# Performance work log

Hardware: AMD Instinct MI355X
Metric: run time of the kernel (lower is better)

Reference implementation:

```python
import jax, jax.numpy as jnp
from jax import lax
import numpy as np

# gate config (matches init_kwargs)
TOP_K = 8
N_GROUP = 8
TOPK_GROUP = 4
ROUTED_SCALING_FACTOR = 2.5
NORM_TOPK_PROB = True


def setup_inputs() -> dict:
    key = jax.random.key(0)
    k1, k2, k3 = jax.random.split(key, 3)
    B, S, H, E = 4, 4096, 4096, 256
    x = jax.random.normal(k1, (B, S, H), dtype=jnp.float32)
    weight = jax.random.normal(k2, (E, H), dtype=jnp.float32) * 0.02
    bias = jax.random.normal(k3, (E,), dtype=jnp.float32) * 0.01
    return {"x": x, "weight": weight, "bias": bias}


def reference(x, weight, bias):
    # gate logits: [B, S, E]
    gates = jnp.einsum('bsh,eh->bse', x, weight)
    scores = jax.nn.sigmoid(gates.astype(jnp.float32))
    orig_scores = scores
    s = scores + bias  # biased scores used only for selection

    B, S, E = s.shape
    if N_GROUP > 1:
        Eg = E // N_GROUP
        sg = s.reshape(B, S, N_GROUP, Eg)
        # group score = sum of top-2 expert scores within each group: [B, S, G]
        group_scores = lax.top_k(sg, 2)[0].sum(axis=-1)
        k_drop = N_GROUP - TOPK_GROUP
        # indices of the k_drop lowest-scoring groups
        drop_idx = lax.top_k(-group_scores, k_drop)[1]  # [B, S, k_drop]
        # keep mask over groups: [B, S, G]
        keep = ~jnp.any(drop_idx[..., :, None] == jnp.arange(N_GROUP), axis=-2)
        sg = jnp.where(keep[..., None], sg, 0.0)  # scatter_ 0.0 on dropped groups
        s = sg.reshape(B, S, E)

    # final top-k over masked, biased scores
    inds = lax.top_k(s, TOP_K)[1]  # [B, S, TOP_K]
    sel = jnp.take_along_axis(orig_scores, inds, axis=-1)  # unbiased scores
    if TOP_K > 1 and NORM_TOPK_PROB:
        sel = sel / (sel.sum(axis=-1, keepdims=True) + 1e-20)
    sel = sel * ROUTED_SCALING_FACTOR
    return (inds, sel)
```

## Files before the change

### kernel.cpp

```cpp
#include <hip/hip_runtime.h>
#include <hip/hip_bf16.h>
#include <math.h>
#include <stdint.h>

#define HDIM   4096
#define NEXP   256
#define TOPK   8
#define NGRP   8
#define NTOK   16384
#define KSPLIT 2
#define BM     64
#define BK     32
#define KCHUNKS (HDIM/BK)
#define NIT    ((HDIM/KSPLIT)/BK)
#define TAU    2.5e-5f
#define TAUG   5.0e-5f

typedef __attribute__((ext_vector_type(8))) short short8v;
typedef __attribute__((ext_vector_type(4))) float f32x4;

#define WS_WSPLIT  (2ull*NTOK*NEXP*4)
#define WS_CTR     (WS_WSPLIT + 4ull*1024*1024)
#define WS_LIST    (WS_CTR + 256)

__device__ inline void gload_lds16(const void* g, void* l) {
    __builtin_amdgcn_global_load_lds(
        (const __attribute__((address_space(1))) unsigned int*)g,
        (__attribute__((address_space(3))) unsigned int*)l, 16, 0, 0);
}

__device__ inline unsigned rtn16(unsigned u) {
    return (u + 0x7fffu + ((u >> 16) & 1u)) >> 16;
}

__global__ __launch_bounds__(256)
void convert_w(const float* __restrict__ w, unsigned short* __restrict__ wws)
{
    int gid  = blockIdx.x * 256 + threadIdx.x;
    int e    = gid >> 9;
    int cell = gid & 511;
    int kc = cell >> 2, kb = cell & 3;
    const float* src = w + (size_t)e * HDIM + cell * 8;
    float4 f0 = *(const float4*)src;
    float4 f1 = *(const float4*)(src + 4);
    float fs[8] = {f0.x,f0.y,f0.z,f0.w,f1.x,f1.y,f1.z,f1.w};
    unsigned hw[4], lw[4];
#pragma unroll
    for (int p = 0; p < 4; ++p) {
        unsigned u0 = __float_as_uint(fs[2*p]);
        unsigned u1 = __float_as_uint(fs[2*p+1]);
        unsigned h0 = rtn16(u0), h1 = rtn16(u1);
        float r0 = fs[2*p]   - __uint_as_float(h0 << 16);
        float r1 = fs[2*p+1] - __uint_as_float(h1 << 16);
        unsigned l0 = rtn16(__float_as_uint(r0));
        unsigned l1 = rtn16(__float_as_uint(r1));
        hw[p] = h0 | (h1 << 16);
        lw[p] = l0 | (l1 << 16);
    }
    size_t bh = ((size_t)(kc*2 + 0)*4 + kb)*2048 + e*8;
    size_t blo= ((size_t)(kc*2 + 1)*4 + kb)*2048 + e*8;
    *(uint4*)&wws[bh]  = make_uint4(hw[0],hw[1],hw[2],hw[3]);
    *(uint4*)&wws[blo] = make_uint4(lw[0],lw[1],lw[2],lw[3]);
}

__global__ __launch_bounds__(256, 2)
void gate_gemm(const float* __restrict__ x, const unsigned short* __restrict__ wws,
               float* __restrict__ partials)
{
    __shared__ uint4 ldsv[2560];
    char* lds = (char*)ldsv;
    const int t = threadIdx.x;
    const int wid = t >> 6, lane = t & 63;
    const int mb = blockIdx.x & 255, ks = blockIdx.x >> 8;
    const size_t m0 = (size_t)mb * BM;
    const int frow = lane & 15, fkb = lane >> 4;
    const int srow = t & 63, skb = t >> 6;

    f32x4 acc[4][4];
#pragma unroll
    for (int m = 0; m < 4; ++m)
#pragma unroll
        for (int n = 0; n < 4; ++n) acc[m][n] = (f32x4){0.f,0.f,0.f,0.f};

    const float* xrow = x + (m0 + srow) * HDIM + ks * (HDIM/KSPLIT) + skb * 8;
    const char* wbase = (const char*)wws + (size_t)(ks * (KCHUNKS/KSPLIT)) * 32768;

    float4 xa = *(const float4*)(xrow);
    float4 xb = *(const float4*)(xrow + 4);

    for (int it = 0; it < NIT; ++it) {
        __syncthreads();
        {
            float fs[8] = {xa.x,xa.y,xa.z,xa.w,xb.x,xb.y,xb.z,xb.w};
            unsigned hw[4], lw[4];
#pragma unroll
            for (int p = 0; p < 4; ++p) {
                unsigned u0 = __float_as_uint(fs[2*p]);
                unsigned u1 = __float_as_uint(fs[2*p+1]);
                hw[p] = (u0 >> 16) | (u1 & 0xffff0000u);
                float r0 = fs[2*p]   - __uint_as_float(u0 & 0xffff0000u);
                float r1 = fs[2*p+1] - __uint_as_float(u1 & 0xffff0000u);
                unsigned l0 = rtn16(__float_as_uint(r0));
                unsigned l1 = rtn16(__float_as_uint(r1));
                lw[p] = l0 | (l1 << 16);
            }
            *(uint4*)&lds[skb*1024 + srow*16]        = make_uint4(hw[0],hw[1],hw[2],hw[3]);
            *(uint4*)&lds[4096 + skb*1024 + srow*16] = make_uint4(lw[0],lw[1],lw[2],lw[3]);
        }
        {
            const char* wsrc = wbase + (size_t)it * 32768;
#pragma unroll
            for (int j = 0; j < 8; ++j) {
                int chunk = wid * 8 + j;
                gload_lds16(wsrc + chunk*1024 + lane*16, &lds[8192 + chunk*1024]);
            }
        }
        __syncthreads();
        if (it + 1 < NIT) {
            xa = *(const float4*)(xrow + (it+1)*BK);
            xb = *(const float4*)(xrow + (it+1)*BK + 4);
        }
        short8v ah[4], al[4];
#pragma unroll
        for (int m = 0; m < 4; ++m) {
            ah[m] = *(const short8v*)&lds[        fkb*1024 + (m*16+frow)*16];
            al[m] = *(const short8v*)&lds[4096 +  fkb*1024 + (m*16+frow)*16];
        }
#pragma unroll
        for (int n = 0; n < 4; ++n) {
            int col = wid*64 + n*16 + frow;
            short8v bh = *(const short8v*)&lds[8192 +         fkb*4096 + col*16];
            short8v bl = *(const short8v*)&lds[8192 + 16384 + fkb*4096 + col*16];
#pragma unroll
            for (int m = 0; m < 4; ++m)
                acc[m][n] = __builtin_amdgcn_mfma_f32_16x16x32_bf16(ah[m], bh, acc[m][n], 0,0,0);
#pragma unroll
            for (int m = 0; m < 4; ++m)
                acc[m][n] = __builtin_amdgcn_mfma_f32_16x16x32_bf16(ah[m], bl, acc[m][n], 0,0,0);
#pragma unroll
            for (int m = 0; m < 4; ++m)
                acc[m][n] = __builtin_amdgcn_mfma_f32_16x16x32_bf16(al[m], bh, acc[m][n], 0,0,0);
        }
    }
    float* pb = partials + (size_t)ks * NTOK * NEXP;
#pragma unroll
    for (int m = 0; m < 4; ++m)
#pragma unroll
        for (int n = 0; n < 4; ++n) {
            int col = wid*64 + n*16 + (lane & 15);
#pragma unroll
            for (int r = 0; r < 4; ++r) {
                size_t row = m0 + m*16 + (lane >> 4)*4 + r;
                pb[row*NEXP + col] = acc[m][n][r];
            }
        }
}

__device__ void wave_gate_topk(float* gb , float* ss ,
                               const float* __restrict__ bias, int lane, size_t tok,
                               float* __restrict__ oIdx, float* __restrict__ oVal,
                               unsigned* flagCtr, int* flagList)
{
    float bv[4]; int ce[4];
#pragma unroll
    for (int j = 0; j < 4; ++j) {
        int e = lane + 64*j;
        float s = 1.f / (1.f + expf(-gb[e]));
        float b = s + bias[e];
        ss[e] = s; gb[e] = b;
        bv[j] = b; ce[j] = e;
    }
    int g = lane >> 3;
    float4 gv = *(const float4*)(gb + g*32 + (lane & 7)*4);
    float a1 = fmaxf(gv.x,gv.y), a2 = fminf(gv.x,gv.y);
    float b1 = fmaxf(gv.z,gv.w), b2 = fminf(gv.z,gv.w);
    float m1 = fmaxf(a1,b1);
    float m2 = fmaxf(fminf(a1,b1), fmaxf(a2,b2));
#pragma unroll
    for (int off = 1; off < 8; off <<= 1) {
        float om1 = __shfl_xor(m1, off), om2 = __shfl_xor(m2, off);
        float n1 = fmaxf(m1, om1);
        float n2 = fmaxf(fminf(m1, om1), fmaxf(m2, om2));
        m1 = n1; m2 = n2;
    }
    float gs = m1 + m2;
    float gsc[8];
#pragma unroll
    for (int i = 0; i < 8; ++i) gsc[i] = __shfl(gs, i*8);
    unsigned dropped = 0; float lastdrop = 0.f;
#pragma unroll
    for (int itd = 0; itd < 4; ++itd) {
        float mn = 1e38f; int mi = 0;
#pragma unroll
        for (int i = 0; i < 8; ++i)
            if (!((dropped >> i) & 1) && gsc[i] < mn) { mn = gsc[i]; mi = i; }
        dropped |= 1u << mi; lastdrop = mn;
    }
    float minkeep = 1e38f;
#pragma unroll
    for (int i = 0; i < 8; ++i)
        if (!((dropped >> i) & 1)) minkeep = fminf(minkeep, gsc[i]);
    float gmargin = minkeep - lastdrop;

    float cv[4];
#pragma unroll
    for (int j = 0; j < 4; ++j)
        cv[j] = ((dropped >> (ce[j] >> 5)) & 1) ? 0.0f : bv[j];

    float vals[9]; int ind[9];
#pragma unroll
    for (int r = 0; r < 9; ++r) {
        float lv = -1e38f; int li = 0x7fffffff;
#pragma unroll
        for (int j = 0; j < 4; ++j)
            if (cv[j] > lv || (cv[j] == lv && ce[j] < li)) { lv = cv[j]; li = ce[j]; }
#pragma unroll
        for (int off = 32; off >= 1; off >>= 1) {
            float ov = __shfl_xor(lv, off);
            int   oi = __shfl_xor(li, off);
            if (ov > lv || (ov == lv && oi < li)) { lv = ov; li = oi; }
        }
        vals[r] = lv; ind[r] = li;
#pragma unroll
        for (int j = 0; j < 4; ++j)
            if (ce[j] == li) cv[j] = -1e38f;
    }
    float mingap = 1e38f;
#pragma unroll
    for (int r = 0; r < 8; ++r) mingap = fminf(mingap, vals[r] - vals[r+1]);

    int myi = 0;
#pragma unroll
    for (int r = 0; r < 8; ++r) if (lane == r) myi = ind[r];
    float sv = (lane < 8) ? ss[myi] : 0.f;
    float sum = sv;
#pragma unroll
    for (int off = 1; off < 8; off <<= 1) sum += __shfl_xor(sum, off);
    if (lane < 8) {
        oIdx[tok*8 + lane] = (float)myi;
        oVal[tok*8 + lane] = sv / (sum + 1e-20f) * 2.5f;
    }
    if (flagCtr && lane == 0 && (mingap < TAU || gmargin < TAUG)) {
        unsigned p = atomicAdd(flagCtr, 1u);
        flagList[p] = (int)tok;
    }
}

__global__ __launch_bounds__(256, 4)
void gate_topk(const float* __restrict__ partials, const float* __restrict__ bias,
               float* __restrict__ oIdx, float* __restrict__ oVal,
               unsigned* ctr, int* list)
{
    __shared__ float gb[4][256];
    __shared__ float ss[4][256];
    int wid = threadIdx.x >> 6, lane = threadIdx.x & 63;
    size_t tok = (size_t)blockIdx.x * 4 + wid;
    const float* p0 = partials + tok * NEXP;
    const float* p1 = partials + (size_t)NTOK * NEXP + tok * NEXP;
#pragma unroll
    for (int j = 0; j < 4; ++j) {
        int e = lane + 64*j;
        gb[wid][e] = p0[e] + p1[e];
    }
    wave_gate_topk(gb[wid], ss[wid], bias, lane, tok, oIdx, oVal, ctr, list);
}

__global__ __launch_bounds__(256, 2)
void gate_refine(const float* __restrict__ x, const float* __restrict__ w,
                 const float* __restrict__ bias,
                 float* __restrict__ oIdx, float* __restrict__ oVal,
                 const unsigned* __restrict__ ctr, const int* __restrict__ list)
{
    __shared__ float gb[4][256];
    __shared__ float ss[4][256];
    int nf = (int)*ctr;
    int nb = (nf + 3) >> 2;
    int e = threadIdx.x;
    int wid = threadIdx.x >> 6, lane = threadIdx.x & 63;
    for (int batch = blockIdx.x; batch < nb; batch += gridDim.x) {
        int tcount = nf - batch*4; if (tcount > 4) tcount = 4;
        int tk[4];
#pragma unroll
        for (int i = 0; i < 4; ++i) {
            int ii = i < tcount ? i : tcount - 1;
            tk[i] = list[batch*4 + ii];
        }
        const float* wr = w + (size_t)e * HDIM;
        const float* x0 = x + (size_t)tk[0] * HDIM;
        const float* x1 = x + (size_t)tk[1] * HDIM;
        const float* x2 = x + (size_t)tk[2] * HDIM;
        const float* x3 = x + (size_t)tk[3] * HDIM;
        float a0=0.f, a1=0.f, a2=0.f, a3=0.f;
        for (int k = 0; k < HDIM; k += 4) {
            float4 wv = *(const float4*)(wr + k);
            float4 v0 = *(const float4*)(x0 + k);
            float4 v1 = *(const float4*)(x1 + k);
            float4 v2 = *(const float4*)(x2 + k);
            float4 v3 = *(const float4*)(x3 + k);
            a0 += wv.x*v0.x + wv.y*v0.y + wv.z*v0.z + wv.w*v0.w;
            a1 += wv.x*v1.x + wv.y*v1.y + wv.z*v1.z + wv.w*v1.w;
            a2 += wv.x*v2.x + wv.y*v2.y + wv.z*v2.z + wv.w*v2.w;
            a3 += wv.x*v3.x + wv.y*v3.y + wv.z*v3.z + wv.w*v3.w;
        }
        __syncthreads();
        gb[0][e] = a0; gb[1][e] = a1; gb[2][e] = a2; gb[3][e] = a3;
        __syncthreads();
        if (wid < tcount)
            wave_gate_topk(gb[wid], ss[wid], bias, lane, (size_t)tk[wid],
                           oIdx, oVal, nullptr, nullptr);
    }
}

extern "C" void kernel_launch(void* const* d_in, const int* in_sizes, int n_in,
                              void* d_out, int out_size, void* d_ws, size_t ws_size,
                              hipStream_t stream) {
    const float* x    = (const float*)d_in[0];
    const float* w    = (const float*)d_in[1];
    const float* bias = (const float*)d_in[2];
    const int ntok = in_sizes[0] / HDIM;

    char* ws = (char*)d_ws;
    float* partials      = (float*)ws;
    unsigned short* wws  = (unsigned short*)(ws + WS_WSPLIT);
    unsigned* ctr        = (unsigned*)(ws + WS_CTR);
    int* list            = (int*)(ws + WS_LIST);
    float* oIdx = (float*)d_out;
    float* oVal = (float*)d_out + (size_t)ntok * TOPK;

    hipMemsetAsync(ctr, 0, 4, stream);
    convert_w <<<512, 256, 0, stream>>>(w, wws);
    gate_gemm <<<(ntok/BM) * KSPLIT, 256, 0, stream>>>(x, wws, partials);
    gate_topk <<<ntok/4, 256, 0, stream>>>(partials, bias, oIdx, oVal, ctr, list);
    gate_refine<<<256, 256, 0, stream>>>(x, w, bias, oIdx, oVal, ctr, list);
}
```

Baseline: 782.3 us.

## Use 512-thread GEMM blocks, swizzled LDS layouts, and per-token refine kernel

The gate GEMM moves to 512-thread blocks where each wave covers 32 experts instead of 64. The weight and activation LDS layouts are reordered so fragment reads are contiguous, and the activation high part now uses round-to-nearest instead of truncation. The refine kernel switches from four tokens per block with one thread per expert to one token per block staged in LDS, using wave-level reductions over experts across more blocks. These changes aim for higher occupancy and better memory access, at the cost of more W traffic per flagged token in refine and extra barriers per K-step.

```diff
diff --git a/kernel.cpp b/kernel.cpp
--- a/kernel.cpp
+++ b/kernel.cpp
@@ -57,13 +57,15 @@
         hw[p] = h0 | (h1 << 16);
         lw[p] = l0 | (l1 << 16);
     }
-    size_t bh = ((size_t)(kc*2 + 0)*4 + kb)*2048 + e*8;
-    size_t blo= ((size_t)(kc*2 + 1)*4 + kb)*2048 + e*8;
-    *(uint4*)&wws[bh]  = make_uint4(hw[0],hw[1],hw[2],hw[3]);
-    *(uint4*)&wws[blo] = make_uint4(lw[0],lw[1],lw[2],lw[3]);
-}
-
-__global__ __launch_bounds__(256, 2)
+    int lane = (e & 15) * 4 + kb;
+    int c    = e >> 4;
+    size_t bh = ((size_t)(kc*2 + 0)*16 + c)*512 + lane*8;
+    size_t bl = ((size_t)(kc*2 + 1)*16 + c)*512 + lane*8;
+    *(uint4*)&wws[bh] = make_uint4(hw[0],hw[1],hw[2],hw[3]);
+    *(uint4*)&wws[bl] = make_uint4(lw[0],lw[1],lw[2],lw[3]);
+}
+
+__global__ __launch_bounds__(512, 4)
 void gate_gemm(const float* __restrict__ x, const unsigned short* __restrict__ wws,
                float* __restrict__ partials)
 {
@@ -74,63 +76,63 @@
     const int mb = blockIdx.x & 255, ks = blockIdx.x >> 8;
     const size_t m0 = (size_t)mb * BM;
     const int frow = lane & 15, fkb = lane >> 4;
-    const int srow = t & 63, skb = t >> 6;
-
-    f32x4 acc[4][4];
+
+    f32x4 acc[4][2];
 #pragma unroll
     for (int m = 0; m < 4; ++m)
 #pragma unroll
-        for (int n = 0; n < 4; ++n) acc[m][n] = (f32x4){0.f,0.f,0.f,0.f};
-
+        for (int n = 0; n < 2; ++n) acc[m][n] = (f32x4){0.f,0.f,0.f,0.f};
+
+    const int srow = t >> 2, skb = t & 3;
     const float* xrow = x + (m0 + srow) * HDIM + ks * (HDIM/KSPLIT) + skb * 8;
-    const char* wbase = (const char*)wws + (size_t)(ks * (KCHUNKS/KSPLIT)) * 32768;
-
-    float4 xa = *(const float4*)(xrow);
-    float4 xb = *(const float4*)(xrow + 4);
+    const char* wbase = (const char*)wws + (size_t)ks * (KCHUNKS/KSPLIT) * 32768;
+
+    float4 xa, xb;
+    if (t < 256) { xa = *(const float4*)(xrow); xb = *(const float4*)(xrow + 4); }
 
     for (int it = 0; it < NIT; ++it) {
         __syncthreads();
-        {
+        if (t < 256) {
             float fs[8] = {xa.x,xa.y,xa.z,xa.w,xb.x,xb.y,xb.z,xb.w};
             unsigned hw[4], lw[4];
 #pragma unroll
             for (int p = 0; p < 4; ++p) {
                 unsigned u0 = __float_as_uint(fs[2*p]);
                 unsigned u1 = __float_as_uint(fs[2*p+1]);
-                hw[p] = (u0 >> 16) | (u1 & 0xffff0000u);
-                float r0 = fs[2*p]   - __uint_as_float(u0 & 0xffff0000u);
-                float r1 = fs[2*p+1] - __uint_as_float(u1 & 0xffff0000u);
-                unsigned l0 = rtn16(__float_as_uint(r0));
-                unsigned l1 = rtn16(__float_as_uint(r1));
-                lw[p] = l0 | (l1 << 16);
-            }
-            *(uint4*)&lds[skb*1024 + srow*16]        = make_uint4(hw[0],hw[1],hw[2],hw[3]);
-            *(uint4*)&lds[4096 + skb*1024 + srow*16] = make_uint4(lw[0],lw[1],lw[2],lw[3]);
+                unsigned h0 = rtn16(u0), h1 = rtn16(u1);
+                float r0 = fs[2*p]   - __uint_as_float(h0 << 16);
+                float r1 = fs[2*p+1] - __uint_as_float(h1 << 16);
+                lw[p] = rtn16(__float_as_uint(r0)) | (rtn16(__float_as_uint(r1)) << 16);
+                hw[p] = h0 | (h1 << 16);
+            }
+            *(uint4*)&lds[       t*16] = make_uint4(hw[0],hw[1],hw[2],hw[3]);
+            *(uint4*)&lds[4096 + t*16] = make_uint4(lw[0],lw[1],lw[2],lw[3]);
         }
         {
             const char* wsrc = wbase + (size_t)it * 32768;
 #pragma unroll
-            for (int j = 0; j < 8; ++j) {
-                int chunk = wid * 8 + j;
-                gload_lds16(wsrc + chunk*1024 + lane*16, &lds[8192 + chunk*1024]);
-            }
-        }
-        __syncthreads();
-        if (it + 1 < NIT) {
+            for (int j = 0; j < 4; ++j) {
+                int idx = wid * 4 + j;
+                gload_lds16(wsrc + idx*1024 + lane*16, &lds[8192 + idx*1024]);
+            }
+        }
+        __syncthreads();
+        if (t < 256 && it + 1 < NIT) {
             xa = *(const float4*)(xrow + (it+1)*BK);
             xb = *(const float4*)(xrow + (it+1)*BK + 4);
         }
         short8v ah[4], al[4];
 #pragma unroll
         for (int m = 0; m < 4; ++m) {
-            ah[m] = *(const short8v*)&lds[        fkb*1024 + (m*16+frow)*16];
-            al[m] = *(const short8v*)&lds[4096 +  fkb*1024 + (m*16+frow)*16];
-        }
-#pragma unroll
-        for (int n = 0; n < 4; ++n) {
-            int col = wid*64 + n*16 + frow;
-            short8v bh = *(const short8v*)&lds[8192 +         fkb*4096 + col*16];
-            short8v bl = *(const short8v*)&lds[8192 + 16384 + fkb*4096 + col*16];
+            int ao = (m*16 + frow)*64 + fkb*16;
+            ah[m] = *(const short8v*)&lds[ao];
+            al[m] = *(const short8v*)&lds[4096 + ao];
+        }
+#pragma unroll
+        for (int n = 0; n < 2; ++n) {
+            int bo = 8192 + (wid*2 + n)*1024 + (frow*4 + fkb)*16;
+            short8v bh = *(const short8v*)&lds[bo];
+            short8v bl = *(const short8v*)&lds[bo + 16384];
 #pragma unroll
             for (int m = 0; m < 4; ++m)
                 acc[m][n] = __builtin_amdgcn_mfma_f32_16x16x32_bf16(ah[m], bh, acc[m][n], 0,0,0);
@@ -146,8 +148,8 @@
 #pragma unroll
     for (int m = 0; m < 4; ++m)
 #pragma unroll
-        for (int n = 0; n < 4; ++n) {
-            int col = wid*64 + n*16 + (lane & 15);
+        for (int n = 0; n < 2; ++n) {
+            int col = wid*32 + n*16 + (lane & 15);
 #pragma unroll
             for (int r = 0; r < 4; ++r) {
                 size_t row = m0 + m*16 + (lane >> 4)*4 + r;
@@ -265,48 +267,48 @@
     wave_gate_topk(gb[wid], ss[wid], bias, lane, tok, oIdx, oVal, ctr, list);
 }
 
-__global__ __launch_bounds__(256, 2)
+__global__ __launch_bounds__(256, 4)
 void gate_refine(const float* __restrict__ x, const float* __restrict__ w,
                  const float* __restrict__ bias,
                  float* __restrict__ oIdx, float* __restrict__ oVal,
                  const unsigned* __restrict__ ctr, const int* __restrict__ list)
 {
-    __shared__ float gb[4][256];
-    __shared__ float ss[4][256];
-    int nf = (int)*ctr;
-    int nb = (nf + 3) >> 2;
-    int e = threadIdx.x;
-    int wid = threadIdx.x >> 6, lane = threadIdx.x & 63;
-    for (int batch = blockIdx.x; batch < nb; batch += gridDim.x) {
-        int tcount = nf - batch*4; if (tcount > 4) tcount = 4;
-        int tk[4];
-#pragma unroll
-        for (int i = 0; i < 4; ++i) {
-            int ii = i < tcount ? i : tcount - 1;
-            tk[i] = list[batch*4 + ii];
-        }
-        const float* wr = w + (size_t)e * HDIM;
-        const float* x0 = x + (size_t)tk[0] * HDIM;
-        const float* x1 = x + (size_t)tk[1] * HDIM;
-        const float* x2 = x + (size_t)tk[2] * HDIM;
-        const float* x3 = x + (size_t)tk[3] * HDIM;
-        float a0=0.f, a1=0.f, a2=0.f, a3=0.f;
-        for (int k = 0; k < HDIM; k += 4) {
-            float4 wv = *(const float4*)(wr + k);
-            float4 v0 = *(const float4*)(x0 + k);
-            float4 v1 = *(const float4*)(x1 + k);
-            float4 v2 = *(const float4*)(x2 + k);
-            float4 v3 = *(const float4*)(x3 + k);
-            a0 += wv.x*v0.x + wv.y*v0.y + wv.z*v0.z + wv.w*v0.w;
-            a1 += wv.x*v1.x + wv.y*v1.y + wv.z*v1.z + wv.w*v1.w;
-            a2 += wv.x*v2.x + wv.y*v2.y + wv.z*v2.z + wv.w*v2.w;
-            a3 += wv.x*v3.x + wv.y*v3.y + wv.z*v3.z + wv.w*v3.w;
-        }
-        __syncthreads();
-        gb[0][e] = a0; gb[1][e] = a1; gb[2][e] = a2; gb[3][e] = a3;
-        __syncthreads();
-        if (wid < tcount)
-            wave_gate_topk(gb[wid], ss[wid], bias, lane, (size_t)tk[wid],
+    __shared__ float xsh[HDIM];
+    __shared__ float gb[NEXP];
+    __shared__ float ss[NEXP];
+    const int nf = (int)*ctr;
+    const int wid = threadIdx.x >> 6, lane = threadIdx.x & 63;
+
+    for (int fi = blockIdx.x; fi < nf; fi += gridDim.x) {
+        int tok = list[fi];
+        __syncthreads();
+        const float4* xsrc = (const float4*)(x + (size_t)tok * HDIM);
+        float4* xd = (float4*)xsh;
+        for (int j = threadIdx.x; j < HDIM/4; j += 256) xd[j] = xsrc[j];
+        __syncthreads();
+
+        for (int e8 = 0; e8 < 64; e8 += 2) {
+            int e0 = wid*64 + e8;
+            const float4* w0 = (const float4*)(w + (size_t)e0 * HDIM);
+            const float4* w1 = (const float4*)(w + (size_t)(e0+1) * HDIM);
+            float a0 = 0.f, a1 = 0.f;
+            for (int k = lane; k < HDIM/4; k += 64) {
+                float4 xv = xd[k];
+                float4 wa = w0[k];
+                float4 wb = w1[k];
+                a0 += wa.x*xv.x + wa.y*xv.y + wa.z*xv.z + wa.w*xv.w;
+                a1 += wb.x*xv.x + wb.y*xv.y + wb.z*xv.z + wb.w*xv.w;
+            }
+#pragma unroll
+            for (int off = 32; off >= 1; off >>= 1) {
+                a0 += __shfl_xor(a0, off);
+                a1 += __shfl_xor(a1, off);
+            }
+            if (lane == 0) { gb[e0] = a0; gb[e0+1] = a1; }
+        }
+        __syncthreads();
+        if (wid == 0)
+            wave_gate_topk(gb, ss, bias, lane, (size_t)tok,
                            oIdx, oVal, nullptr, nullptr);
     }
 }
@@ -328,8 +330,8 @@
     float* oVal = (float*)d_out + (size_t)ntok * TOPK;
 
     hipMemsetAsync(ctr, 0, 4, stream);
-    convert_w <<<512, 256, 0, stream>>>(w, wws);
-    gate_gemm <<<(ntok/BM) * KSPLIT, 256, 0, stream>>>(x, wws, partials);
-    gate_topk <<<ntok/4, 256, 0, stream>>>(partials, bias, oIdx, oVal, ctr, list);
-    gate_refine<<<256, 256, 0, stream>>>(x, w, bias, oIdx, oVal, ctr, list);
-}
+    convert_w  <<<512, 256, 0, stream>>>(w, wws);
+    gate_gemm  <<<(ntok/BM) * KSPLIT, 512, 0, stream>>>(x, wws, partials);
+    gate_topk  <<<ntok/4, 256, 0, stream>>>(partials, bias, oIdx, oVal, ctr, list);
+    gate_refine<<<1024, 256, 0, stream>>>(x, w, bias, oIdx, oVal, ctr, list);
+}
```

Measured after the change: 704.7 us. 1.11x faster.
